# Performance work log

Measured on AMD Instinct MI355X. Metric: run time of the kernel, lower is better.

Reference implementation:

```python
import jax, jax.numpy as jnp
import numpy as np
from functools import partial

NUM_CLUSTERS = 64
KMEANS_ITERS = 10  # fixed Lloyd iterations standing in for sklearn's converged fit


def _assign(points, centers):
    # points: [M, D], centers: [K, D] -> labels [M]
    # squared L2 distance via expansion; the -|x|^2 term is constant per point
    d = jnp.sum(centers * centers, axis=1)[None, :] - 2.0 * (points @ centers.T)
    return jnp.argmin(d, axis=1)


def _kmeans_fit_predict(points, num_clusters, iters):
    # Deterministic init: first K points (fixed-seed sklearn stand-in).
    centers0 = points[:num_clusters]

    def step(centers, _):
        labels = _assign(points, centers)
        sums = jax.ops.segment_sum(points, labels, num_segments=num_clusters)
        counts = jax.ops.segment_sum(jnp.ones((points.shape[0],), points.dtype),
                                     labels, num_segments=num_clusters)
        new_centers = jnp.where(counts[:, None] > 0, sums / jnp.maximum(counts, 1.0)[:, None], centers)
        return new_centers, None

    centers, _ = jax.lax.scan(step, centers0, None, length=iters)
    labels = _assign(points, centers)
    return labels, centers


def setup_inputs() -> dict:
    key = jax.random.key(0)
    k1, k2, k3 = jax.random.split(key, 3)
    B, N, D = 16, 4096, 384
    x = jax.random.normal(k1, (B, N, D), dtype=jnp.float32)
    # nn.Linear(feature_dim, feature_dim): weight [out, in], bias [out]
    scale = 1.0 / np.sqrt(D)
    W = jax.random.uniform(k2, (D, D), dtype=jnp.float32, minval=-scale, maxval=scale)
    b = jax.random.uniform(k3, (D,), dtype=jnp.float32, minval=-scale, maxval=scale)
    return {"x": x, "W": W, "b": b}


def reference(x, W, b):
    B, N, D = x.shape
    x_flat = jax.lax.stop_gradient(x.reshape(-1, D))  # torch does .detach() before kmeans
    labels, centers = _kmeans_fit_predict(x_flat, NUM_CLUSTERS, KMEANS_ITERS)
    clustered = centers[labels].reshape(B, N, D)
    return clustered @ W.T + b
```

## Files before the change

### kernel.cpp

```cpp
#include <hip/hip_runtime.h>

#define P_TOT 65536
#define DIM   384
#define KCL   64
#define ITERS 10
#define BPTS  128
#define NSB   8
#define BK    32
#define NKT   (DIM / BK)
#define LDA   128
#define LDB   68


__global__ __launch_bounds__(384) void init_kernel(const float* __restrict__ x,
                                                   float* __restrict__ centers,
                                                   float* __restrict__ cnorm,
                                                   float* __restrict__ cnt,
                                                   float* __restrict__ sums) {
    __shared__ float red[384];
    const int c = blockIdx.x, t = threadIdx.x;
    float v = x[(size_t)c * DIM + t];
    centers[(size_t)c * DIM + t] = v;
#pragma unroll
    for (int b = 0; b < NSB; ++b) sums[(size_t)b * KCL * DIM + (size_t)c * DIM + t] = 0.f;
    if (t == 0) cnt[c] = 0.f;
    red[t] = v * v;
    __syncthreads();
    if (t < 128) red[t] = red[t] + red[t + 128] + red[t + 256];
    __syncthreads();
    for (int s = 64; s > 0; s >>= 1) {
        if (t < s) red[t] += red[t + s];
        __syncthreads();
    }
    if (t == 0) cnorm[c] = red[0];
}

#define GEMM_ARGMIN_BODY(X, CENTERS, CNORM)                                          \
    const int t    = threadIdx.x;                                                    \
    const int cg   = t & 15;                              \
    const int pg   = t >> 4;                         \
    const int p0   = blockIdx.x * BPTS;                                              \
    const int sar  = t >> 2;                               \
    const int sak  = (t & 3) * 4;           \
    const int sbr  = t >> 3;                                \
    const int sbk  = (t & 7) * 4;                    \
    if (t < KCL) scn[t] = (CNORM)[t];                                                \
    float acc[4][4];                                                                 \
    _Pragma("unroll")                                                                \
    for (int i = 0; i < 4; ++i)                                                      \
        _Pragma("unroll")                                                            \
        for (int j = 0; j < 4; ++j) acc[i][j] = 0.f;                                 \
    const float* xrow = (X) + (size_t)(p0 + sar) * DIM;                              \
    const float* crow = (CENTERS) + (size_t)sbr * DIM;                               \
    float4 ra0 = *(const float4*)(xrow + sak);                                       \
    float4 ra1 = *(const float4*)(xrow + sak + 16);                                  \
    float4 rb  = *(const float4*)(crow + sbk);                                       \
    for (int kt = 0; kt < NKT; ++kt) {                                               \
        const int cur = kt & 1;                                                      \
        At[cur][sak + 0][sar] = ra0.x;  At[cur][sak + 1][sar] = ra0.y;               \
        At[cur][sak + 2][sar] = ra0.z;  At[cur][sak + 3][sar] = ra0.w;               \
        At[cur][sak + 16][sar] = ra1.x; At[cur][sak + 17][sar] = ra1.y;              \
        At[cur][sak + 18][sar] = ra1.z; At[cur][sak + 19][sar] = ra1.w;              \
        Bt[cur][sbk + 0][sbr] = rb.x;   Bt[cur][sbk + 1][sbr] = rb.y;                \
        Bt[cur][sbk + 2][sbr] = rb.z;   Bt[cur][sbk + 3][sbr] = rb.w;                \
        if (kt + 1 < NKT) {                        \
            const int k0 = (kt + 1) * BK;                                            \
            ra0 = *(const float4*)(xrow + k0 + sak);                                 \
            ra1 = *(const float4*)(xrow + k0 + sak + 16);                            \
            rb  = *(const float4*)(crow + k0 + sbk);                                 \
        }                                                                            \
        __syncthreads();                                \
        _Pragma("unroll")                                                            \
        for (int kk = 0; kk < BK; ++kk) {                                            \
            float4 a4 = *(const float4*)&At[cur][kk][pg * 4];                        \
            float4 b4 = *(const float4*)&Bt[cur][kk][cg * 4];                        \
            const float av[4] = {a4.x, a4.y, a4.z, a4.w};                            \
            const float bv[4] = {b4.x, b4.y, b4.z, b4.w};                            \
            _Pragma("unroll")                                                        \
            for (int i = 0; i < 4; ++i)                                              \
                _Pragma("unroll")                                                    \
                for (int j = 0; j < 4; ++j) acc[i][j] += av[i] * bv[j];              \
        }                                                                            \
    }                                                                                \
    {                                                                                \
        float cn[4];                                                                 \
        _Pragma("unroll")                                                            \
        for (int j = 0; j < 4; ++j) cn[j] = scn[cg * 4 + j];                         \
        _Pragma("unroll")                                                            \
        for (int i = 0; i < 4; ++i) {                                                \
            float bvv = 3.4e38f; int bc = 0;                                         \
            _Pragma("unroll")                                                        \
            for (int j = 0; j < 4; ++j) {                                            \
                float d = cn[j] - 2.0f * acc[i][j];                                  \
                if (d < bvv) { bvv = d; bc = cg * 4 + j; }                           \
            }                                                                        \
            _Pragma("unroll")                                                        \
            for (int m = 1; m < 16; m <<= 1) {       \
                float ov = __shfl_xor(bvv, m, 64);                                   \
                int   oc = __shfl_xor(bc, m, 64);                                    \
                if (ov < bvv || (ov == bvv && oc < bc)) { bvv = ov; bc = oc; }       \
            }                                                                        \
            if (cg == 0) lab[pg * 4 + i] = bc;             \
        }                                                                            \
    }                                                                                \
    __syncthreads();

__global__ __launch_bounds__(512, 4) void fused_kernel(const float* __restrict__ x,
                                                       const float* __restrict__ centers,
                                                       const float* __restrict__ cnorm,
                                                       float* __restrict__ sums,
                                                       float* __restrict__ cnt) {
    __shared__ float At[2][BK][LDA];
    __shared__ float Bt[2][BK][LDB];
    __shared__ float scn[KCL];
    __shared__ int   lab[BPTS];
    __shared__ int   lcnt[KCL];
    __shared__ int   lstart[KCL + 1];
    __shared__ int   lcur[KCL];
    __shared__ int   order[BPTS];

    if (threadIdx.x < KCL) lcnt[threadIdx.x] = 0;

    GEMM_ARGMIN_BODY(x, centers, cnorm)

    int myl = -1;
    if (t < BPTS) {
        myl = lab[t];
        atomicAdd(&lcnt[myl], 1);
    }
    __syncthreads();
    if (t < 64) {
        int v = lcnt[t];
        int s = v;
#pragma unroll
        for (int d = 1; d < 64; d <<= 1) {
            int u = __shfl_up(s, d, 64);
            if (t >= d) s += u;
        }
        lstart[t] = s - v;
        lcur[t] = s - v;
        if (t == 63) lstart[64] = s;
    }
    __syncthreads();
    if (t < BPTS) {
        int pos = atomicAdd(&lcur[myl], 1);
        order[pos] = t;
    }
    __syncthreads();

    if (t < DIM) {
        const float* xb = x + (size_t)p0 * DIM;
        float* sb = sums + (size_t)(blockIdx.x & (NSB - 1)) * KCL * DIM;
        int   curc = lab[order[0]];
        float run  = 0.f;
        for (int j = 0; j < BPTS; ++j) {
            const int p = order[j];
            const int c = lab[p];
            if (c != curc) {
                atomicAdd(&sb[curc * DIM + t], run);
                run = 0.f;
                curc = c;
            }
            run += xb[(size_t)p * DIM + t];
        }
        atomicAdd(&sb[curc * DIM + t], run);
    }
    if (t < KCL && lcnt[t] > 0) atomicAdd(&cnt[t], (float)lcnt[t]);
}

__global__ __launch_bounds__(512, 4) void label_kernel(const float* __restrict__ x,
                                                       const float* __restrict__ centers,
                                                       const float* __restrict__ cnorm,
                                                       int* __restrict__ labs) {
    __shared__ float At[2][BK][LDA];
    __shared__ float Bt[2][BK][LDB];
    __shared__ float scn[KCL];
    __shared__ int   lab[BPTS];

    GEMM_ARGMIN_BODY(x, centers, cnorm)

    if (t < BPTS) labs[p0 + t] = lab[t];
}

__global__ __launch_bounds__(384) void update_kernel(float* __restrict__ sums,
                                                     float* __restrict__ cnt,
                                                     float* __restrict__ centers,
                                                     float* __restrict__ cnorm) {
    __shared__ float red[384];
    const int c = blockIdx.x, t = threadIdx.x;
    float s = 0.f;
#pragma unroll
    for (int b = 0; b < NSB; ++b) {
        const size_t idx = (size_t)b * KCL * DIM + (size_t)c * DIM + t;
        s += sums[idx];
        sums[idx] = 0.f;
    }
    float n = cnt[c];
    float oldv = centers[(size_t)c * DIM + t];
    float nc = (n > 0.f) ? (s / n) : oldv;
    centers[(size_t)c * DIM + t] = nc;
    red[t] = nc * nc;
    __syncthreads();
    if (t == 0) cnt[c] = 0.f;
    if (t < 128) red[t] = red[t] + red[t + 128] + red[t + 256];
    __syncthreads();
    for (int st = 64; st > 0; st >>= 1) {
        if (t < st) red[t] += red[t + st];
        __syncthreads();
    }
    if (t == 0) cnorm[c] = red[0];
}

__global__ __launch_bounds__(384) void cw_kernel(const float* __restrict__ centers,
                                                 const float* __restrict__ W,
                                                 const float* __restrict__ b,
                                                 float* __restrict__ CW) {
    __shared__ float cs[DIM];
    const int c = blockIdx.x, j = threadIdx.x;
    cs[j] = centers[(size_t)c * DIM + j];
    __syncthreads();
    float acc = b[j];
    const float* wr = W + (size_t)j * DIM;
    for (int d4 = 0; d4 < 96; ++d4) {
        float4 v = *(const float4*)(wr + d4 * 4);
        acc += cs[d4 * 4 + 0] * v.x + cs[d4 * 4 + 1] * v.y
             + cs[d4 * 4 + 2] * v.z + cs[d4 * 4 + 3] * v.w;
    }
    CW[(size_t)c * DIM + j] = acc;
}

__global__ __launch_bounds__(256) void gather_kernel(const int* __restrict__ labs,
                                                     const float* __restrict__ CW,
                                                     float* __restrict__ out) {
    __shared__ int lab[32];
    const int t = threadIdx.x;
    const int p0 = blockIdx.x * 32;
    if (t < 32) lab[t] = labs[p0 + t];
    __syncthreads();
    const int pp = t >> 3;
    const int j0 = t & 7;
    const float* src = CW + (size_t)lab[pp] * DIM;
    float* dst = out + (size_t)(p0 + pp) * DIM;
#pragma unroll
    for (int r = 0; r < 12; ++r) {
        const int jg = (r * 8 + j0) * 4;
        *(float4*)(dst + jg) = *(const float4*)(src + jg);
    }
}

extern "C" void kernel_launch(void* const* d_in, const int* in_sizes, int n_in,
                              void* d_out, int out_size, void* d_ws, size_t ws_size,
                              hipStream_t stream) {
    const float* x = (const float*)d_in[0];
    const float* W = (const float*)d_in[1];
    const float* b = (const float*)d_in[2];
    float* out = (float*)d_out;

    float* centers = (float*)d_ws;
    float* cnorm   = centers + KCL * DIM;
    float* cnt     = cnorm + KCL;
    float* CW      = cnt + KCL;
    float* sums    = CW + KCL * DIM;
    int* labs      = (int*)sums;

    init_kernel<<<KCL, 384, 0, stream>>>(x, centers, cnorm, cnt, sums);
    for (int it = 0; it < ITERS; ++it) {
        fused_kernel<<<P_TOT / BPTS, 512, 0, stream>>>(x, centers, cnorm, sums, cnt);
        update_kernel<<<KCL, 384, 0, stream>>>(sums, cnt, centers, cnorm);
    }
    cw_kernel<<<KCL, 384, 0, stream>>>(centers, W, b, CW);
    label_kernel<<<P_TOT / BPTS, 512, 0, stream>>>(x, centers, cnorm, labs);
    gather_kernel<<<P_TOT / 32, 256, 0, stream>>>(labs, CW, out);
}
```

Baseline: 1.227 ms.

## Double points per block, use 8x4 register tiles, and batch scatter loads

Raises points per block from 128 to 256 and gives each thread an 8x4 accumulator tile instead of 4x4. The A tile is now stored row-major, padded, and written with float4 stores in place of scalar transposed writes. The scatter-add loop now prefetches 8 point values and labels before the run-length atomics. The aim is to increase arithmetic intensity per shared-memory load and to hide global-load latency in the scatter. In exchange it uses more registers and LDS, drops the occupancy hint from 4 to 2 blocks, and halves the grid to 256 blocks.

```diff
diff --git a/kernel.cpp b/kernel.cpp
--- a/kernel.cpp
+++ b/kernel.cpp
@@ -4,12 +4,12 @@
 #define DIM   384
 #define KCL   64
 #define ITERS 10
-#define BPTS  128
+#define BPTS  256
 #define NSB   8
 #define BK    32
 #define NKT   (DIM / BK)
-#define LDA   128
-#define LDB   68
+#define LKA   36
+#define LKB   68
 
 
 __global__ __launch_bounds__(384) void init_kernel(const float* __restrict__ x,
@@ -36,50 +36,63 @@
 }
 
 #define GEMM_ARGMIN_BODY(X, CENTERS, CNORM)                                          \
-    const int t    = threadIdx.x;                                                    \
-    const int cg   = t & 15;                              \
-    const int pg   = t >> 4;                         \
-    const int p0   = blockIdx.x * BPTS;                                              \
-    const int sar  = t >> 2;                               \
-    const int sak  = (t & 3) * 4;           \
-    const int sbr  = t >> 3;                                \
-    const int sbk  = (t & 7) * 4;                    \
+    const int t   = threadIdx.x;                                                     \
+    const int cg  = t & 15;                               \
+    const int pg  = t >> 4;                          \
+    const int p0  = blockIdx.x * BPTS;                                               \
+    const int spt = t >> 1;                             \
+    const int sah = (t & 1) * 16;                      \
+    const int sbc = t >> 3;                            \
+    const int sbk = (t & 7) * 4;                \
     if (t < KCL) scn[t] = (CNORM)[t];                                                \
-    float acc[4][4];                                                                 \
+    float acc[8][4];                                                                 \
     _Pragma("unroll")                                                                \
-    for (int i = 0; i < 4; ++i)                                                      \
+    for (int i = 0; i < 8; ++i)                                                      \
         _Pragma("unroll")                                                            \
         for (int j = 0; j < 4; ++j) acc[i][j] = 0.f;                                 \
-    const float* xrow = (X) + (size_t)(p0 + sar) * DIM;                              \
-    const float* crow = (CENTERS) + (size_t)sbr * DIM;                               \
-    float4 ra0 = *(const float4*)(xrow + sak);                                       \
-    float4 ra1 = *(const float4*)(xrow + sak + 16);                                  \
+    const float* xrow = (X) + (size_t)(p0 + spt) * DIM;                              \
+    const float* crow = (CENTERS) + (size_t)sbc * DIM;                               \
+    float4 ra0 = *(const float4*)(xrow + sah);                                       \
+    float4 ra1 = *(const float4*)(xrow + sah + 4);                                   \
+    float4 ra2 = *(const float4*)(xrow + sah + 8);                                   \
+    float4 ra3 = *(const float4*)(xrow + sah + 12);                                  \
     float4 rb  = *(const float4*)(crow + sbk);                                       \
     for (int kt = 0; kt < NKT; ++kt) {                                               \
         const int cur = kt & 1;                                                      \
-        At[cur][sak + 0][sar] = ra0.x;  At[cur][sak + 1][sar] = ra0.y;               \
-        At[cur][sak + 2][sar] = ra0.z;  At[cur][sak + 3][sar] = ra0.w;               \
-        At[cur][sak + 16][sar] = ra1.x; At[cur][sak + 17][sar] = ra1.y;              \
-        At[cur][sak + 18][sar] = ra1.z; At[cur][sak + 19][sar] = ra1.w;              \
-        Bt[cur][sbk + 0][sbr] = rb.x;   Bt[cur][sbk + 1][sbr] = rb.y;                \
-        Bt[cur][sbk + 2][sbr] = rb.z;   Bt[cur][sbk + 3][sbr] = rb.w;                \
+        *(float4*)&At[cur][spt][sah + 0]  = ra0;                                     \
+        *(float4*)&At[cur][spt][sah + 4]  = ra1;                                     \
+        *(float4*)&At[cur][spt][sah + 8]  = ra2;                                     \
+        *(float4*)&At[cur][spt][sah + 12] = ra3;                                     \
+        Bt[cur][sbk + 0][sbc] = rb.x;  Bt[cur][sbk + 1][sbc] = rb.y;                 \
+        Bt[cur][sbk + 2][sbc] = rb.z;  Bt[cur][sbk + 3][sbc] = rb.w;                 \
         if (kt + 1 < NKT) {                        \
             const int k0 = (kt + 1) * BK;                                            \
-            ra0 = *(const float4*)(xrow + k0 + sak);                                 \
-            ra1 = *(const float4*)(xrow + k0 + sak + 16);                            \
+            ra0 = *(const float4*)(xrow + k0 + sah);                                 \
+            ra1 = *(const float4*)(xrow + k0 + sah + 4);                             \
+            ra2 = *(const float4*)(xrow + k0 + sah + 8);                             \
+            ra3 = *(const float4*)(xrow + k0 + sah + 12);                            \
             rb  = *(const float4*)(crow + k0 + sbk);                                 \
         }                                                                            \
-        __syncthreads();                                \
-        _Pragma("unroll")                                                            \
-        for (int kk = 0; kk < BK; ++kk) {                                            \
-            float4 a4 = *(const float4*)&At[cur][kk][pg * 4];                        \
-            float4 b4 = *(const float4*)&Bt[cur][kk][cg * 4];                        \
-            const float av[4] = {a4.x, a4.y, a4.z, a4.w};                            \
-            const float bv[4] = {b4.x, b4.y, b4.z, b4.w};                            \
-            _Pragma("unroll")                                                        \
-            for (int i = 0; i < 4; ++i)                                              \
+        __syncthreads();                  \
+        _Pragma("unroll")                                                            \
+        for (int kq = 0; kq < 8; ++kq) {                                             \
+            float af[8][4];                                                          \
+            _Pragma("unroll")                                                        \
+            for (int i = 0; i < 8; ++i) {                                            \
+                const float4 a4 = *(const float4*)&At[cur][pg * 8 + i][kq * 4];      \
+                af[i][0] = a4.x; af[i][1] = a4.y; af[i][2] = a4.z; af[i][3] = a4.w;  \
+            }                                                                        \
+            _Pragma("unroll")                                                        \
+            for (int kk = 0; kk < 4; ++kk) {                                         \
+                const float4 bf = *(const float4*)&Bt[cur][kq * 4 + kk][cg * 4];     \
                 _Pragma("unroll")                                                    \
-                for (int j = 0; j < 4; ++j) acc[i][j] += av[i] * bv[j];              \
+                for (int i = 0; i < 8; ++i) {                                        \
+                    acc[i][0] += af[i][kk] * bf.x;                                   \
+                    acc[i][1] += af[i][kk] * bf.y;                                   \
+                    acc[i][2] += af[i][kk] * bf.z;                                   \
+                    acc[i][3] += af[i][kk] * bf.w;                                   \
+                }                                                                    \
+            }                                                                        \
         }                                                                            \
     }                                                                                \
     {                                                                                \
@@ -87,31 +100,31 @@
         _Pragma("unroll")                                                            \
         for (int j = 0; j < 4; ++j) cn[j] = scn[cg * 4 + j];                         \
         _Pragma("unroll")                                                            \
-        for (int i = 0; i < 4; ++i) {                                                \
+        for (int i = 0; i < 8; ++i) {                                                \
             float bvv = 3.4e38f; int bc = 0;                                         \
             _Pragma("unroll")                                                        \
             for (int j = 0; j < 4; ++j) {                                            \
                 float d = cn[j] - 2.0f * acc[i][j];                                  \
-                if (d < bvv) { bvv = d; bc = cg * 4 + j; }                           \
+                if (d < bvv) { bvv = d; bc = cg * 4 + j; }      \
             }                                                                        \
             _Pragma("unroll")                                                        \
             for (int m = 1; m < 16; m <<= 1) {       \
-                float ov = __shfl_xor(bvv, m, 64);                                   \
-                int   oc = __shfl_xor(bc, m, 64);                                    \
+                const float ov = __shfl_xor(bvv, m, 64);                             \
+                const int   oc = __shfl_xor(bc, m, 64);                              \
                 if (ov < bvv || (ov == bvv && oc < bc)) { bvv = ov; bc = oc; }       \
             }                                                                        \
-            if (cg == 0) lab[pg * 4 + i] = bc;             \
+            if ((t & 15) == 0) lab[pg * 8 + i] = bc;                                 \
         }                                                                            \
     }                                                                                \
     __syncthreads();
 
-__global__ __launch_bounds__(512, 4) void fused_kernel(const float* __restrict__ x,
+__global__ __launch_bounds__(512, 2) void fused_kernel(const float* __restrict__ x,
                                                        const float* __restrict__ centers,
                                                        const float* __restrict__ cnorm,
                                                        float* __restrict__ sums,
                                                        float* __restrict__ cnt) {
-    __shared__ float At[2][BK][LDA];
-    __shared__ float Bt[2][BK][LDB];
+    __shared__ float At[2][BPTS][LKA];
+    __shared__ float Bt[2][BK][LKB];
     __shared__ float scn[KCL];
     __shared__ int   lab[BPTS];
     __shared__ int   lcnt[KCL];
@@ -153,27 +166,34 @@
         float* sb = sums + (size_t)(blockIdx.x & (NSB - 1)) * KCL * DIM;
         int   curc = lab[order[0]];
         float run  = 0.f;
-        for (int j = 0; j < BPTS; ++j) {
-            const int p = order[j];
-            const int c = lab[p];
-            if (c != curc) {
-                atomicAdd(&sb[curc * DIM + t], run);
-                run = 0.f;
-                curc = c;
+        for (int j0 = 0; j0 < BPTS; j0 += 8) {
+            float v[8]; int cc[8];
+#pragma unroll
+            for (int u = 0; u < 8; ++u) {
+                const int p = order[j0 + u];
+                cc[u] = lab[p];
+                v[u]  = xb[(size_t)p * DIM + t];
             }
-            run += xb[(size_t)p * DIM + t];
+#pragma unroll
+            for (int u = 0; u < 8; ++u) {
+                if (cc[u] != curc) {
+                    atomicAdd(&sb[curc * DIM + t], run);
+                    run = 0.f; curc = cc[u];
+                }
+                run += v[u];
+            }
         }
         atomicAdd(&sb[curc * DIM + t], run);
     }
     if (t < KCL && lcnt[t] > 0) atomicAdd(&cnt[t], (float)lcnt[t]);
 }
 
-__global__ __launch_bounds__(512, 4) void label_kernel(const float* __restrict__ x,
+__global__ __launch_bounds__(512, 2) void label_kernel(const float* __restrict__ x,
                                                        const float* __restrict__ centers,
                                                        const float* __restrict__ cnorm,
                                                        int* __restrict__ labs) {
-    __shared__ float At[2][BK][LDA];
-    __shared__ float Bt[2][BK][LDB];
+    __shared__ float At[2][BPTS][LKA];
+    __shared__ float Bt[2][BK][LKB];
     __shared__ float scn[KCL];
     __shared__ int   lab[BPTS];
 
```

Result: faster. 1.019 ms (-16.9%).
